# Optimization experiments

Hardware: AMD Instinct MI355X
Metric: run time of the kernel (lower is better)

Reference implementation:

```python
import jax, jax.numpy as jnp
import numpy as np

W_RAD = 2  # box-filter radius (init kwarg w)
KSIZE = 2 * W_RAD + 1


def _box_conv3d(x, kernel):
    # x: [B,1,D,H,W], kernel: [1,1,k,k,k]; 'same' padding, stride 1
    return jax.lax.conv_general_dilated(
        x, kernel,
        window_strides=(1, 1, 1),
        padding=[(W_RAD, W_RAD)] * 3,
        dimension_numbers=("NCDHW", "OIDHW", "NCDHW"),
    )


def setup_inputs() -> dict:
    key = jax.random.key(0)
    k1, k2 = jax.random.split(key)
    shape = (2, 1, 160, 160, 160)
    M = jax.random.uniform(k1, shape, dtype=jnp.float32)
    R = jax.random.uniform(k2, shape, dtype=jnp.float32)
    kernel = jnp.ones((1, 1, KSIZE, KSIZE, KSIZE), dtype=jnp.float32) / (KSIZE ** 3)
    return {"M": M, "R": R, "kernel": kernel}


def reference(M, R, kernel):
    M_m = _box_conv3d(M, kernel)
    R_m = _box_conv3d(R, kernel)
    MM_m = _box_conv3d(M * M, kernel)
    RR_m = _box_conv3d(R * R, kernel)
    MR_m = _box_conv3d(M * R, kernel)
    M_var = jnp.sqrt(MM_m - M_m ** 2 + 1e-05)
    R_var = jnp.sqrt(RR_m - R_m ** 2 + 1e-05)
    corr = (MR_m - M_m * R_m) / (M_var * R_var + 1e-05)
    return -jnp.mean(corr)
```

## Files before the change

kernel.cpp:

```cpp
#include <hip/hip_runtime.h>
#include <math.h>

#define Bsz 2
#define Dd 160
#define Hh 160
#define Ww 160
#define TW 32
#define TH 32
#define DCHUNK 16
#define NT 320
#define NCH 5
#define PDIM 48
#define HROWS (TH + 4)
#define NSLICE (DCHUNK + 4)
#define SLICE (Hh * Ww)

__global__ void lncc_zero(float* out) { out[0] = 0.0f; }

__device__ __forceinline__ void bar_lgkm() {
    asm volatile("s_waitcnt lgkmcnt(0)" ::: "memory");
    __builtin_amdgcn_s_barrier();
    asm volatile("" ::: "memory");
}

__global__ __launch_bounds__(NT)
void lncc_main(const float* __restrict__ M,
               const float* __restrict__ R,
               const float* __restrict__ kern,
               float* __restrict__ out)
{
    __shared__ float sw[NCH][TW][PDIM];
    __shared__ float red[NT / 64];

    const int tid = threadIdx.x;
    const int w0 = blockIdx.x * TW;
    const int h0 = blockIdx.y * TH;
    const int b  = blockIdx.z / (Dd / DCHUNK);
    const int d0 = (blockIdx.z % (Dd / DCHUNK)) * DCHUNK;

    const float k0 = kern[0];

    const bool isB = tid < HROWS * 8;
    const int  g   = tid & 7;
    const int  row = tid >> 3;
    const int  gh  = h0 + row - 2;
    const bool hok = isB && gh >= 0 && gh < Hh;
    bool qok[3]; int qoff[3];
#pragma unroll
    for (int k = 0; k < 3; ++k) {
        int gw = w0 - 4 + 4 * (g + k);
        qok[k]  = hok && gw >= 0 && gw <= (Ww - 4);
        qoff[k] = gh * Ww + gw;
    }
    const size_t bbase = (size_t)b * Dd * SLICE;
    const float* Mb = M + bbase;
    const float* Rb = R + bbase;

    float4 cm[3], cr[3];
    auto issue = [&](int s) {
        int dd = d0 - 2 + s;
        bool dok = dd >= 0 && dd < Dd;
        const float* Ms = Mb + (size_t)(dok ? dd : 0) * SLICE;
        const float* Rs = Rb + (size_t)(dok ? dd : 0) * SLICE;
#pragma unroll
        for (int k = 0; k < 3; ++k) {
            bool ok = dok && qok[k];
            cm[k] = ok ? *(const float4*)(Ms + qoff[k]) : make_float4(0.f, 0.f, 0.f, 0.f);
            cr[k] = ok ? *(const float4*)(Rs + qoff[k]) : make_float4(0.f, 0.f, 0.f, 0.f);
        }
    };
    float* swp = &sw[0][g * 4][row + 4 * (g & 3)];

    const bool isC = tid < 256;
    const int  cw  = tid & 31;
    const int  hg  = (tid >> 5) & 7;
    const int  p0  = hg * 4 + 4 * ((cw >> 2) & 3);
    const float* crd = &sw[0][cw][p0];

    float ring[5][NCH][4];
#pragma unroll
    for (int t = 0; t < 5; ++t)
#pragma unroll
        for (int c = 0; c < NCH; ++c)
#pragma unroll
            for (int j = 0; j < 4; ++j) ring[t][c][j] = 0.f;

    float acc = 0.f;
    issue(0);

    for (int s5 = 0; s5 < NSLICE; s5 += 5) {
#pragma unroll
        for (int so = 0; so < 5; ++so) {
            const int s = s5 + so;

            bar_lgkm();

            if (isB) {
                float am[12], ar[12];
                *(float4*)&am[0] = cm[0]; *(float4*)&am[4] = cm[1]; *(float4*)&am[8] = cm[2];
                *(float4*)&ar[0] = cr[0]; *(float4*)&ar[4] = cr[1]; *(float4*)&ar[8] = cr[2];
                float mm[8], rr[8], mr[8];
#pragma unroll
                for (int k = 0; k < 8; ++k) {
                    float a = am[k + 2], r_ = ar[k + 2];
                    mm[k] = a * a; rr[k] = r_ * r_; mr[k] = a * r_;
                }
                float sm  = am[2] + am[3] + am[4] + am[5] + am[6];
                float sr_ = ar[2] + ar[3] + ar[4] + ar[5] + ar[6];
                float smm = mm[0] + mm[1] + mm[2] + mm[3] + mm[4];
                float srr = rr[0] + rr[1] + rr[2] + rr[3] + rr[4];
                float smr = mr[0] + mr[1] + mr[2] + mr[3] + mr[4];
#pragma unroll
                for (int j = 0; j < 4; ++j) {
                    if (j) {
                        sm  += am[j + 6] - am[j + 1];
                        sr_ += ar[j + 6] - ar[j + 1];
                        smm += mm[j + 4] - mm[j - 1];
                        srr += rr[j + 4] - rr[j - 1];
                        smr += mr[j + 4] - mr[j - 1];
                    }
                    float* wp = swp + j * PDIM;
                    wp[0 * TW * PDIM] = sm;
                    wp[1 * TW * PDIM] = sr_;
                    wp[2 * TW * PDIM] = smm;
                    wp[3 * TW * PDIM] = srr;
                    wp[4 * TW * PDIM] = smr;
                }
                if (s + 1 < NSLICE) issue(s + 1);
            }

            bar_lgkm();

            if (isC) {
                float hs[NCH][4];
#pragma unroll
                for (int c = 0; c < NCH; ++c) {
                    float4 A  = *(const float4*)(crd + c * TW * PDIM);
                    float4 Bq = *(const float4*)(crd + c * TW * PDIM + 4);
                    float v0 = A.x, v1 = A.y, v2 = A.z, v3 = A.w;
                    float v4 = Bq.x, v5 = Bq.y, v6 = Bq.z, v7 = Bq.w;
                    hs[c][0] = v0 + v1 + v2 + v3 + v4;
                    hs[c][1] = hs[c][0] + v5 - v0;
                    hs[c][2] = hs[c][1] + v6 - v1;
                    hs[c][3] = hs[c][2] + v7 - v2;
#pragma unroll
                    for (int j = 0; j < 4; ++j) ring[so][c][j] = hs[c][j];
                }
                if (s >= 4) {
#pragma unroll
                    for (int j = 0; j < 4; ++j) {
                        float S[NCH];
#pragma unroll
                        for (int c = 0; c < NCH; ++c)
                            S[c] = ring[0][c][j] + ring[1][c][j] + ring[2][c][j]
                                 + ring[3][c][j] + ring[4][c][j];
                        float Mm  = S[0] * k0;
                        float Rm  = S[1] * k0;
                        float MMm = S[2] * k0;
                        float RRm = S[3] * k0;
                        float MRm = S[4] * k0;
                        float Mv = sqrtf(MMm - Mm * Mm + 1e-5f);
                        float Rv = sqrtf(RRm - Rm * Rm + 1e-5f);
                        acc += (MRm - Mm * Rm) / (Mv * Rv + 1e-5f);
                    }
                }
            }
        }
    }

#pragma unroll
    for (int off = 32; off; off >>= 1) acc += __shfl_down(acc, off, 64);
    if ((tid & 63) == 0) red[tid >> 6] = acc;
    __syncthreads();
    if (tid == 0) {
        float t = red[0] + red[1] + red[2] + red[3] + red[4];
        atomicAdd(out, -t * (1.0f / 8192000.0f));
    }
}

extern "C" void kernel_launch(void* const* d_in, const int* in_sizes, int n_in,
                              void* d_out, int out_size, void* d_ws, size_t ws_size,
                              hipStream_t stream) {
    const float* M = (const float*)d_in[0];
    const float* R = (const float*)d_in[1];
    const float* K = (const float*)d_in[2];
    float* out = (float*)d_out;

    lncc_zero<<<1, 1, 0, stream>>>(out);

    dim3 grid(Ww / TW, Hh / TH, Bsz * (Dd / DCHUNK));
    lncc_main<<<grid, NT, 0, stream>>>(M, R, K, out);
}
```

Before: 136.2 us.

## Double-buffer LDS and register prefetch to overlap B and C phases

Double-buffers the shared-memory stage and the register prefetch so the row-sum phase for slice s runs alongside the column-sum phase for slice s-1. This halves the barriers per slice and prefetches global loads two slices ahead. It also swaps the five-slot ring summation for a running sum with subtract-old-add-new, shrinks the LDS padding and drops the swizzle, and adds launch bounds asking for two blocks per CU. The costs are more registers and LDS, possible LDS bank conflicts from the unswizzled layout, and a running sum that can drift slightly in floating point.

After: 141.9 us. 1.04x slower.

```diff
diff --git a/kernel.cpp b/kernel.cpp
--- a/kernel.cpp
+++ b/kernel.cpp
@@ -1,19 +1,18 @@
 #include <hip/hip_runtime.h>
 #include <math.h>
 
-#define Bsz 2
 #define Dd 160
 #define Hh 160
 #define Ww 160
 #define TW 32
 #define TH 32
 #define DCHUNK 16
+#define NSLICE (DCHUNK + 4)
 #define NT 320
 #define NCH 5
-#define PDIM 48
-#define HROWS (TH + 4)
-#define NSLICE (DCHUNK + 4)
+#define PDIM 36
 #define SLICE (Hh * Ww)
+#define NDC (Dd / DCHUNK)
 
 __global__ void lncc_zero(float* out) { out[0] = 0.0f; }
 
@@ -23,41 +22,39 @@
     asm volatile("" ::: "memory");
 }
 
-__global__ __launch_bounds__(NT)
-void lncc_main(const float* __restrict__ M,
-               const float* __restrict__ R,
-               const float* __restrict__ kern,
-               float* __restrict__ out)
+__global__ __launch_bounds__(NT, 2)
+void lncc_main(const float* __restrict__ M, const float* __restrict__ R,
+               const float* __restrict__ kern, float* __restrict__ out)
 {
-    __shared__ float sw[NCH][TW][PDIM];
+    __shared__ float sw[2][NCH][TW][PDIM];
     __shared__ float red[NT / 64];
 
     const int tid = threadIdx.x;
     const int w0 = blockIdx.x * TW;
     const int h0 = blockIdx.y * TH;
-    const int b  = blockIdx.z / (Dd / DCHUNK);
-    const int d0 = (blockIdx.z % (Dd / DCHUNK)) * DCHUNK;
-
+    const int b  = blockIdx.z / NDC;
+    const int d0 = (blockIdx.z % NDC) * DCHUNK;
     const float k0 = kern[0];
 
-    const bool isB = tid < HROWS * 8;
-    const int  g   = tid & 7;
-    const int  row = tid >> 3;
-    const int  gh  = h0 + row - 2;
+    const bool isB = tid < (TH + 4) * 8;
+    const int g   = tid & 7;
+    const int row = tid >> 3;
+    const int gh  = h0 + row - 2;
     const bool hok = isB && gh >= 0 && gh < Hh;
     bool qok[3]; int qoff[3];
 #pragma unroll
     for (int k = 0; k < 3; ++k) {
         int gw = w0 - 4 + 4 * (g + k);
-        qok[k]  = hok && gw >= 0 && gw <= (Ww - 4);
+        qok[k]  = hok && gw >= 0 && gw <= Ww - 4;
         qoff[k] = gh * Ww + gw;
     }
-    const size_t bbase = (size_t)b * Dd * SLICE;
-    const float* Mb = M + bbase;
-    const float* Rb = R + bbase;
+    const size_t bb = (size_t)b * Dd * SLICE;
+    const float* Mb = M + bb;
+    const float* Rb = R + bb;
 
-    float4 cm[3], cr[3];
-    auto issue = [&](int s) {
+    float4 cm[2][3], cr[2][3];
+
+    auto issue = [&](int s, int pp) {
         int dd = d0 - 2 + s;
         bool dok = dd >= 0 && dd < Dd;
         const float* Ms = Mb + (size_t)(dok ? dd : 0) * SLICE;
@@ -65,106 +62,113 @@
 #pragma unroll
         for (int k = 0; k < 3; ++k) {
             bool ok = dok && qok[k];
-            cm[k] = ok ? *(const float4*)(Ms + qoff[k]) : make_float4(0.f, 0.f, 0.f, 0.f);
-            cr[k] = ok ? *(const float4*)(Rs + qoff[k]) : make_float4(0.f, 0.f, 0.f, 0.f);
+            cm[pp][k] = ok ? *(const float4*)(Ms + qoff[k]) : make_float4(0.f, 0.f, 0.f, 0.f);
+            cr[pp][k] = ok ? *(const float4*)(Rs + qoff[k]) : make_float4(0.f, 0.f, 0.f, 0.f);
         }
     };
-    float* swp = &sw[0][g * 4][row + 4 * (g & 3)];
+
+    auto bphase = [&](int sp) {
+        if (!isB) return;
+        float am[12], ar[12];
+        *(float4*)&am[0] = cm[sp][0]; *(float4*)&am[4] = cm[sp][1]; *(float4*)&am[8] = cm[sp][2];
+        *(float4*)&ar[0] = cr[sp][0]; *(float4*)&ar[4] = cr[sp][1]; *(float4*)&ar[8] = cr[sp][2];
+        float mm[8], rr[8], mr[8];
+#pragma unroll
+        for (int k2 = 0; k2 < 8; ++k2) {
+            float a = am[k2 + 2], r_ = ar[k2 + 2];
+            mm[k2] = a * a; rr[k2] = r_ * r_; mr[k2] = a * r_;
+        }
+        float sm  = am[2] + am[3] + am[4] + am[5] + am[6];
+        float sr_ = ar[2] + ar[3] + ar[4] + ar[5] + ar[6];
+        float smm = mm[0] + mm[1] + mm[2] + mm[3] + mm[4];
+        float srr = rr[0] + rr[1] + rr[2] + rr[3] + rr[4];
+        float smr = mr[0] + mr[1] + mr[2] + mr[3] + mr[4];
+#pragma unroll
+        for (int j = 0; j < 4; ++j) {
+            if (j) {
+                sm  += am[j + 6] - am[j + 1];
+                sr_ += ar[j + 6] - ar[j + 1];
+                smm += mm[j + 4] - mm[j - 1];
+                srr += rr[j + 4] - rr[j - 1];
+                smr += mr[j + 4] - mr[j - 1];
+            }
+            const int wq = 4 * g + j;
+            sw[sp][0][wq][row] = sm;
+            sw[sp][1][wq][row] = sr_;
+            sw[sp][2][wq][row] = smm;
+            sw[sp][3][wq][row] = srr;
+            sw[sp][4][wq][row] = smr;
+        }
+    };
 
     const bool isC = tid < 256;
-    const int  cw  = tid & 31;
-    const int  hg  = (tid >> 5) & 7;
-    const int  p0  = hg * 4 + 4 * ((cw >> 2) & 3);
-    const float* crd = &sw[0][cw][p0];
+    const int cw = tid & 31;
+    const int hg = (tid >> 5) & 7;
 
+    float S[NCH][4];
     float ring[5][NCH][4];
 #pragma unroll
-    for (int t = 0; t < 5; ++t)
+    for (int c = 0; c < NCH; ++c)
 #pragma unroll
-        for (int c = 0; c < NCH; ++c)
+        for (int j = 0; j < 4; ++j) {
+            S[c][j] = 0.f;
 #pragma unroll
-            for (int j = 0; j < 4; ++j) ring[t][c][j] = 0.f;
+            for (int t = 0; t < 5; ++t) ring[t][c][j] = 0.f;
+        }
+    float acc = 0.f;
 
-    float acc = 0.f;
-    issue(0);
+    auto cphase = [&](int cs, int cp, int slot) {
+        if (!isC) return;
+        const float* base = &sw[cp][0][cw][hg * 4];
+        float4 A  = *(const float4*)(base);
+        float4 Bq = *(const float4*)(base + 4);
+#pragma unroll
+        for (int c = 0; c < NCH; ++c) {
+            float4 An, Bn;
+            if (c < 4) {
+                An = *(const float4*)(base + (c + 1) * TW * PDIM);
+                Bn = *(const float4*)(base + (c + 1) * TW * PDIM + 4);
+            }
+            float t0 = A.x + A.y + A.z + A.w + Bq.x;
+            float t1 = t0 + Bq.y - A.x;
+            float t2 = t1 + Bq.z - A.y;
+            float t3 = t2 + Bq.w - A.z;
+            S[c][0] += t0 - ring[slot][c][0]; ring[slot][c][0] = t0;
+            S[c][1] += t1 - ring[slot][c][1]; ring[slot][c][1] = t1;
+            S[c][2] += t2 - ring[slot][c][2]; ring[slot][c][2] = t2;
+            S[c][3] += t3 - ring[slot][c][3]; ring[slot][c][3] = t3;
+            A = An; Bq = Bn;
+        }
+        if (cs >= 4) {
+#pragma unroll
+            for (int j = 0; j < 4; ++j) {
+                float Mm  = S[0][j] * k0, Rm = S[1][j] * k0;
+                float MMm = S[2][j] * k0, RRm = S[3][j] * k0, MRm = S[4][j] * k0;
+                float Mv = sqrtf(MMm - Mm * Mm + 1e-5f);
+                float Rv = sqrtf(RRm - Rm * Rm + 1e-5f);
+                acc += (MRm - Mm * Rm) / (Mv * Rv + 1e-5f);
+            }
+        }
+    };
 
-    for (int s5 = 0; s5 < NSLICE; s5 += 5) {
+    issue(0, 0);
+    issue(1, 1);
+    bphase(0);
+    issue(2, 0);
+
+    for (int m = 0; m < 2; ++m) {
 #pragma unroll
-        for (int so = 0; so < 5; ++so) {
-            const int s = s5 + so;
-
+        for (int k = 0; k < 10; ++k) {
+            const int s  = m * 10 + k + 1;
+            const int sp = (k + 1) & 1;
+            const int cp = k & 1;
+            const int sl = k % 5;
             bar_lgkm();
-
-            if (isB) {
-                float am[12], ar[12];
-                *(float4*)&am[0] = cm[0]; *(float4*)&am[4] = cm[1]; *(float4*)&am[8] = cm[2];
-                *(float4*)&ar[0] = cr[0]; *(float4*)&ar[4] = cr[1]; *(float4*)&ar[8] = cr[2];
-                float mm[8], rr[8], mr[8];
-#pragma unroll
-                for (int k = 0; k < 8; ++k) {
-                    float a = am[k + 2], r_ = ar[k + 2];
-                    mm[k] = a * a; rr[k] = r_ * r_; mr[k] = a * r_;
-                }
-                float sm  = am[2] + am[3] + am[4] + am[5] + am[6];
-                float sr_ = ar[2] + ar[3] + ar[4] + ar[5] + ar[6];
-                float smm = mm[0] + mm[1] + mm[2] + mm[3] + mm[4];
-                float srr = rr[0] + rr[1] + rr[2] + rr[3] + rr[4];
-                float smr = mr[0] + mr[1] + mr[2] + mr[3] + mr[4];
-#pragma unroll
-                for (int j = 0; j < 4; ++j) {
-                    if (j) {
-                        sm  += am[j + 6] - am[j + 1];
-                        sr_ += ar[j + 6] - ar[j + 1];
-                        smm += mm[j + 4] - mm[j - 1];
-                        srr += rr[j + 4] - rr[j - 1];
-                        smr += mr[j + 4] - mr[j - 1];
-                    }
-                    float* wp = swp + j * PDIM;
-                    wp[0 * TW * PDIM] = sm;
-                    wp[1 * TW * PDIM] = sr_;
-                    wp[2 * TW * PDIM] = smm;
-                    wp[3 * TW * PDIM] = srr;
-                    wp[4 * TW * PDIM] = smr;
-                }
-                if (s + 1 < NSLICE) issue(s + 1);
+            if (s <= NSLICE - 1) {
+                bphase(sp);
+                if (s + 2 <= NSLICE - 1) issue(s + 2, sp);
             }
-
-            bar_lgkm();
-
-            if (isC) {
-                float hs[NCH][4];
-#pragma unroll
-                for (int c = 0; c < NCH; ++c) {
-                    float4 A  = *(const float4*)(crd + c * TW * PDIM);
-                    float4 Bq = *(const float4*)(crd + c * TW * PDIM + 4);
-                    float v0 = A.x, v1 = A.y, v2 = A.z, v3 = A.w;
-                    float v4 = Bq.x, v5 = Bq.y, v6 = Bq.z, v7 = Bq.w;
-                    hs[c][0] = v0 + v1 + v2 + v3 + v4;
-                    hs[c][1] = hs[c][0] + v5 - v0;
-                    hs[c][2] = hs[c][1] + v6 - v1;
-                    hs[c][3] = hs[c][2] + v7 - v2;
-#pragma unroll
-                    for (int j = 0; j < 4; ++j) ring[so][c][j] = hs[c][j];
-                }
-                if (s >= 4) {
-#pragma unroll
-                    for (int j = 0; j < 4; ++j) {
-                        float S[NCH];
-#pragma unroll
-                        for (int c = 0; c < NCH; ++c)
-                            S[c] = ring[0][c][j] + ring[1][c][j] + ring[2][c][j]
-                                 + ring[3][c][j] + ring[4][c][j];
-                        float Mm  = S[0] * k0;
-                        float Rm  = S[1] * k0;
-                        float MMm = S[2] * k0;
-                        float RRm = S[3] * k0;
-                        float MRm = S[4] * k0;
-                        float Mv = sqrtf(MMm - Mm * Mm + 1e-5f);
-                        float Rv = sqrtf(RRm - Rm * Rm + 1e-5f);
-                        acc += (MRm - Mm * Rm) / (Mv * Rv + 1e-5f);
-                    }
-                }
-            }
+            cphase(s - 1, cp, sl);
         }
     }
 
@@ -188,6 +192,6 @@
 
     lncc_zero<<<1, 1, 0, stream>>>(out);
 
-    dim3 grid(Ww / TW, Hh / TH, Bsz * (Dd / DCHUNK));
+    dim3 grid(Ww / TW, Hh / TH, 2 * NDC);
     lncc_main<<<grid, NT, 0, stream>>>(M, R, K, out);
 }
```

## Shrink depth chunk, use running depth sums, and target two blocks per CU

Applied to the files above, without the earlier changes.

Depth chunk drops from 16 to 10 slices, so the grid grows from 500 to 800 blocks for better CU fill, at the cost of a larger halo overhead (14 slices loaded per 10 output slices). The depth-direction sum is now a running sum that subtracts the evicted ring entry instead of re-adding five ring slots, and launch bounds ask for 2 blocks per CU. The LDS padding swizzle is removed (PDIM 48 to 36), which shrinks shared memory but may bring back bank conflicts. Running sums can also accumulate floating-point drift across slices.

Result: slower. 159.3 us (+17.0%).

```diff
diff --git a/kernel.cpp b/kernel.cpp
--- a/kernel.cpp
+++ b/kernel.cpp
@@ -1,18 +1,17 @@
 #include <hip/hip_runtime.h>
 #include <math.h>
 
-#define Bsz 2
 #define Dd 160
 #define Hh 160
 #define Ww 160
 #define TW 32
 #define TH 32
-#define DCHUNK 16
+#define DCHUNK 10
 #define NT 320
 #define NCH 5
-#define PDIM 48
-#define HROWS (TH + 4)
+#define PDIM 36
 #define NSLICE (DCHUNK + 4)
+#define NDC (Dd / DCHUNK)
 #define SLICE (Hh * Ww)
 
 __global__ void lncc_zero(float* out) { out[0] = 0.0f; }
@@ -23,7 +22,7 @@
     asm volatile("" ::: "memory");
 }
 
-__global__ __launch_bounds__(NT)
+__global__ __launch_bounds__(NT, 2)
 void lncc_main(const float* __restrict__ M,
                const float* __restrict__ R,
                const float* __restrict__ kern,
@@ -35,12 +34,12 @@
     const int tid = threadIdx.x;
     const int w0 = blockIdx.x * TW;
     const int h0 = blockIdx.y * TH;
-    const int b  = blockIdx.z / (Dd / DCHUNK);
-    const int d0 = (blockIdx.z % (Dd / DCHUNK)) * DCHUNK;
+    const int b  = blockIdx.z >> 4;
+    const int d0 = (blockIdx.z & 15) * DCHUNK;
 
     const float k0 = kern[0];
 
-    const bool isB = tid < HROWS * 8;
+    const bool isB = tid < (TH + 4) * 8;
     const int  g   = tid & 7;
     const int  row = tid >> 3;
     const int  gh  = h0 + row - 2;
@@ -69,29 +68,32 @@
             cr[k] = ok ? *(const float4*)(Rs + qoff[k]) : make_float4(0.f, 0.f, 0.f, 0.f);
         }
     };
-    float* swp = &sw[0][g * 4][row + 4 * (g & 3)];
+    float* swp = &sw[0][g * 4][row];
 
     const bool isC = tid < 256;
     const int  cw  = tid & 31;
     const int  hg  = (tid >> 5) & 7;
-    const int  p0  = hg * 4 + 4 * ((cw >> 2) & 3);
-    const float* crd = &sw[0][cw][p0];
+    const float* crd = &sw[0][cw][4 * hg];
 
+    float S[NCH][4];
     float ring[5][NCH][4];
 #pragma unroll
-    for (int t = 0; t < 5; ++t)
+    for (int c = 0; c < NCH; ++c)
 #pragma unroll
-        for (int c = 0; c < NCH; ++c)
+        for (int j = 0; j < 4; ++j) {
+            S[c][j] = 0.f;
 #pragma unroll
-            for (int j = 0; j < 4; ++j) ring[t][c][j] = 0.f;
+            for (int t = 0; t < 5; ++t) ring[t][c][j] = 0.f;
+        }
 
     float acc = 0.f;
     issue(0);
 
-    for (int s5 = 0; s5 < NSLICE; s5 += 5) {
+    for (int s5 = 0; s5 < 15; s5 += 5) {
 #pragma unroll
         for (int so = 0; so < 5; ++so) {
             const int s = s5 + so;
+            if (s >= NSLICE) break;
 
             bar_lgkm();
 
@@ -132,33 +134,24 @@
             bar_lgkm();
 
             if (isC) {
-                float hs[NCH][4];
 #pragma unroll
                 for (int c = 0; c < NCH; ++c) {
                     float4 A  = *(const float4*)(crd + c * TW * PDIM);
                     float4 Bq = *(const float4*)(crd + c * TW * PDIM + 4);
-                    float v0 = A.x, v1 = A.y, v2 = A.z, v3 = A.w;
-                    float v4 = Bq.x, v5 = Bq.y, v6 = Bq.z, v7 = Bq.w;
-                    hs[c][0] = v0 + v1 + v2 + v3 + v4;
-                    hs[c][1] = hs[c][0] + v5 - v0;
-                    hs[c][2] = hs[c][1] + v6 - v1;
-                    hs[c][3] = hs[c][2] + v7 - v2;
-#pragma unroll
-                    for (int j = 0; j < 4; ++j) ring[so][c][j] = hs[c][j];
+                    float t0 = A.x + A.y + A.z + A.w + Bq.x;
+                    float t1 = t0 + Bq.y - A.x;
+                    float t2 = t1 + Bq.z - A.y;
+                    float t3 = t2 + Bq.w - A.z;
+                    S[c][0] += t0 - ring[so][c][0]; ring[so][c][0] = t0;
+                    S[c][1] += t1 - ring[so][c][1]; ring[so][c][1] = t1;
+                    S[c][2] += t2 - ring[so][c][2]; ring[so][c][2] = t2;
+                    S[c][3] += t3 - ring[so][c][3]; ring[so][c][3] = t3;
                 }
                 if (s >= 4) {
 #pragma unroll
                     for (int j = 0; j < 4; ++j) {
-                        float S[NCH];
-#pragma unroll
-                        for (int c = 0; c < NCH; ++c)
-                            S[c] = ring[0][c][j] + ring[1][c][j] + ring[2][c][j]
-                                 + ring[3][c][j] + ring[4][c][j];
-                        float Mm  = S[0] * k0;
-                        float Rm  = S[1] * k0;
-                        float MMm = S[2] * k0;
-                        float RRm = S[3] * k0;
-                        float MRm = S[4] * k0;
+                        float Mm  = S[0][j] * k0, Rm = S[1][j] * k0;
+                        float MMm = S[2][j] * k0, RRm = S[3][j] * k0, MRm = S[4][j] * k0;
                         float Mv = sqrtf(MMm - Mm * Mm + 1e-5f);
                         float Rv = sqrtf(RRm - Rm * Rm + 1e-5f);
                         acc += (MRm - Mm * Rm) / (Mv * Rv + 1e-5f);
@@ -188,6 +181,6 @@
 
     lncc_zero<<<1, 1, 0, stream>>>(out);
 
-    dim3 grid(Ww / TW, Hh / TH, Bsz * (Dd / DCHUNK));
+    dim3 grid(Ww / TW, Hh / TH, 2 * NDC);
     lncc_main<<<grid, NT, 0, stream>>>(M, R, K, out);
 }
```
